# Performance work log

Hardware: AMD Instinct MI355X
Metric: run time of the kernel (lower is better)

## Reference

```python
import jax, jax.numpy as jnp
import numpy as np

B, C_IMG, H, W = 16, 512, 32, 32
C_AUD, K_LEN, N_HEADS = 512, 256, 8
HEAD_DIM = C_AUD // N_HEADS
EPS = 1e-5


def setup_inputs() -> dict:
    key = jax.random.key(0)
    ks = jax.random.split(key, 12)
    s_img = 1.0 / np.sqrt(C_IMG)
    s_aud = 1.0 / np.sqrt(C_AUD)
    return {
        "img_feat": jax.random.normal(ks[0], (B, C_IMG, H, W), jnp.float32),
        "audio_feat": jax.random.normal(ks[1], (B, K_LEN, C_AUD), jnp.float32),
        "Wq": jax.random.uniform(ks[2], (C_IMG, C_AUD), jnp.float32, -s_img, s_img),
        "bq": jnp.zeros((C_AUD,), jnp.float32),
        "Wk": jax.random.uniform(ks[3], (C_AUD, C_AUD), jnp.float32, -s_aud, s_aud),
        "bk": jnp.zeros((C_AUD,), jnp.float32),
        "Wv": jax.random.uniform(ks[4], (C_AUD, C_AUD), jnp.float32, -s_aud, s_aud),
        "bv": jnp.zeros((C_AUD,), jnp.float32),
        "Wo": jax.random.uniform(ks[5], (C_AUD, C_IMG), jnp.float32, -s_aud, s_aud),
        "bo": jnp.zeros((C_IMG,), jnp.float32),
        "gamma": jnp.ones((C_IMG,), jnp.float32),
        "beta": jnp.zeros((C_IMG,), jnp.float32),
    }


def reference(img_feat, audio_feat, Wq, bq, Wk, bk, Wv, bv, Wo, bo, gamma, beta):
    b, c, h, w = img_feat.shape
    # b c h w -> b (h w) c
    img_seq = img_feat.reshape(b, c, h * w).transpose(0, 2, 1)
    q = img_seq @ Wq + bq                      # [b, q, C_AUD]
    k = audio_feat @ Wk + bk                   # [b, k, C_AUD]
    v = audio_feat @ Wv + bv
    # split heads: b s (h d) -> b h s d
    def split(x):
        bs, s, _ = x.shape
        return x.reshape(bs, s, N_HEADS, HEAD_DIM).transpose(0, 2, 1, 3)
    qh, kh, vh = split(q), split(k), split(v)
    scale = HEAD_DIM ** -0.5
    scores = jnp.einsum('bhqd,bhkd->bhqk', qh, kh) * scale
    weights = jax.nn.softmax(scores, axis=-1)
    attn = jnp.einsum('bhqk,bhkd->bhqd', weights, vh)
    attn = attn.transpose(0, 2, 1, 3).reshape(b, h * w, C_AUD)
    proj = attn @ Wo + bo                      # [b, q, C_IMG]
    y = img_seq + proj
    mu = jnp.mean(y, axis=-1, keepdims=True)
    var = jnp.mean((y - mu) ** 2, axis=-1, keepdims=True)
    y = (y - mu) * jax.lax.rsqrt(var + EPS) * gamma + beta
    # b (h w) c -> b c h w
    return y.transpose(0, 2, 1).reshape(b, c, h, w)
```

## Files before the change

kernel.cpp:

```cpp
#include <hip/hip_runtime.h>
#include <cstddef>

#define B_SZ 16
#define HW 1024
#define CCH 512
#define K_LEN 256
#define N_HEADS 8
#define EPS 1e-5f

typedef __bf16 bf16;
typedef bf16 bf16x8 __attribute__((ext_vector_type(8)));
typedef bf16 bf16x4 __attribute__((ext_vector_type(4)));
typedef float f32x4 __attribute__((ext_vector_type(4)));

__device__ __forceinline__ void gl_lds16(const bf16* g, bf16* l) {
    __builtin_amdgcn_global_load_lds(
        (const __attribute__((address_space(1))) void*)g,
        (__attribute__((address_space(3))) void*)l, 16, 0, 0);
}

__global__ __launch_bounds__(256) void transpose_cast_img(
    const float* __restrict__ src, bf16* __restrict__ dst)
{
    const int b  = blockIdx.z;
    const int s0 = blockIdx.x * 64;
    const int c0 = blockIdx.y * 64;
    __shared__ bf16 T[64][72];
    const int tid = threadIdx.x;
    {
        const int r = tid >> 2, cs = (tid & 3) << 4;
        const float* sp = src + ((size_t)b * CCH + c0 + r) * HW + s0 + cs;
        #pragma unroll
        for (int i = 0; i < 4; ++i) {
            float4 f = *(const float4*)(sp + i * 4);
            T[r][cs + i*4 + 0] = (bf16)f.x;
            T[r][cs + i*4 + 1] = (bf16)f.y;
            T[r][cs + i*4 + 2] = (bf16)f.z;
            T[r][cs + i*4 + 3] = (bf16)f.w;
        }
    }
    __syncthreads();
    {
        const int ss = tid >> 2, ks = (tid & 3) << 4;
        bf16x8 a, b8;
        #pragma unroll
        for (int j = 0; j < 8; ++j) { a[j] = T[ks + j][ss]; b8[j] = T[ks + 8 + j][ss]; }
        bf16* dp = dst + ((size_t)b * HW + s0 + ss) * CCH + c0 + ks;
        *(bf16x8*)dp = a;
        *(bf16x8*)(dp + 8) = b8;
    }
}

__global__ __launch_bounds__(256) void transpose_cast_w(
    const float* __restrict__ Wq, const float* __restrict__ Wk,
    const float* __restrict__ Wv, const float* __restrict__ Wo,
    bf16* __restrict__ dst)
{
    const int w = blockIdx.z;
    const float* src = (w == 0) ? Wq : (w == 1) ? Wk : (w == 2) ? Wv : Wo;
    const int n0 = blockIdx.x * 64;
    const int k0 = blockIdx.y * 64;
    __shared__ bf16 T[64][72];
    const int tid = threadIdx.x;
    {
        const int r = tid >> 2, cs = (tid & 3) << 4;
        const float* sp = src + (size_t)(k0 + r) * CCH + n0 + cs;
        #pragma unroll
        for (int i = 0; i < 4; ++i) {
            float4 f = *(const float4*)(sp + i * 4);
            T[r][cs + i*4 + 0] = (bf16)f.x;
            T[r][cs + i*4 + 1] = (bf16)f.y;
            T[r][cs + i*4 + 2] = (bf16)f.z;
            T[r][cs + i*4 + 3] = (bf16)f.w;
        }
    }
    __syncthreads();
    {
        const int nn = tid >> 2, ks = (tid & 3) << 4;
        bf16x8 a, b8;
        #pragma unroll
        for (int j = 0; j < 8; ++j) { a[j] = T[ks + j][nn]; b8[j] = T[ks + 8 + j][nn]; }
        bf16* dp = dst + (size_t)w * CCH * CCH + (size_t)(n0 + nn) * CCH + k0 + ks;
        *(bf16x8*)dp = a;
        *(bf16x8*)(dp + 8) = b8;
    }
}

__global__ __launch_bounds__(256) void cast_audio(
    const float* __restrict__ src, bf16* __restrict__ dst)
{
    const size_t i = ((size_t)blockIdx.x * 256 + threadIdx.x) * 8;
    float4 a = *(const float4*)(src + i);
    float4 b = *(const float4*)(src + i + 4);
    bf16x8 o;
    o[0] = (bf16)a.x; o[1] = (bf16)a.y; o[2] = (bf16)a.z; o[3] = (bf16)a.w;
    o[4] = (bf16)b.x; o[5] = (bf16)b.y; o[6] = (bf16)b.z; o[7] = (bf16)b.w;
    *(bf16x8*)(dst + i) = o;
}

__global__ __launch_bounds__(256) void gemm_bf16_mfma(
    const bf16* __restrict__ A, const bf16* __restrict__ Bt,
    const float* __restrict__ bias, bf16* __restrict__ out)
{
    const int tid  = threadIdx.x;
    const int wave = tid >> 6, lane = tid & 63;
    const int m0 = blockIdx.x * 128;
    const int n0 = blockIdx.y * 128;
    const int l15 = lane & 15, quad = lane >> 4;
    const int wm = (wave >> 1) * 64, wn = (wave & 1) * 64;

    __shared__ bf16 As[128 * 32];
    __shared__ bf16 Bs[128 * 32];

    const int r16 = lane >> 2;
    const int ks  = (lane & 3) * 8;

    f32x4 acc[4][4];
    #pragma unroll
    for (int i = 0; i < 4; ++i)
        #pragma unroll
        for (int j = 0; j < 4; ++j)
            acc[i][j] = (f32x4){0.f, 0.f, 0.f, 0.f};

    for (int k0 = 0; k0 < 512; k0 += 32) {
        #pragma unroll
        for (int i = 0; i < 2; ++i) {
            const int c = wave * 2 + i;
            gl_lds16(A  + (size_t)(m0 + c * 16 + r16) * 512 + k0 + ks, &As[c * 512]);
            gl_lds16(Bt + (size_t)(n0 + c * 16 + r16) * 512 + k0 + ks, &Bs[c * 512]);
        }
        __syncthreads();
        bf16x8 af[4], bfr[4];
        #pragma unroll
        for (int i = 0; i < 4; ++i)
            af[i] = *(const bf16x8*)&As[(wm + i * 16 + l15) * 32 + quad * 8];
        #pragma unroll
        for (int j = 0; j < 4; ++j)
            bfr[j] = *(const bf16x8*)&Bs[(wn + j * 16 + l15) * 32 + quad * 8];
        #pragma unroll
        for (int i = 0; i < 4; ++i)
            #pragma unroll
            for (int j = 0; j < 4; ++j)
                acc[i][j] = __builtin_amdgcn_mfma_f32_16x16x32_bf16(bfr[j], af[i], acc[i][j], 0, 0, 0);
        __syncthreads();
    }

    #pragma unroll
    for (int j = 0; j < 4; ++j) {
        const int gn = n0 + wn + j * 16 + quad * 4;
        const float4 bv4 = *(const float4*)(bias + gn);
        const float bb[4] = {bv4.x, bv4.y, bv4.z, bv4.w};
        #pragma unroll
        for (int i = 0; i < 4; ++i) {
            const int gm = m0 + wm + i * 16 + l15;
            bf16x4 ov;
            #pragma unroll
            for (int r = 0; r < 4; ++r) ov[r] = (bf16)(acc[i][j][r] + bb[r]);
            *(bf16x4*)(out + (size_t)gm * 512 + gn) = ov;
        }
    }
}

__global__ __launch_bounds__(256) void gemm_kv_mfma(
    const bf16* __restrict__ A, const bf16* __restrict__ Bt,
    const float* __restrict__ bk, const float* __restrict__ bv,
    bf16* __restrict__ khout, bf16* __restrict__ vtout)
{
    const int tid  = threadIdx.x;
    const int wave = tid >> 6, lane = tid & 63;
    const int m0 = blockIdx.x * 128;
    const int n0 = blockIdx.y * 128;
    const int l15 = lane & 15, quad = lane >> 4;
    const int wm = (wave >> 1) * 64, wn = (wave & 1) * 64;

    __shared__ bf16 As[128 * 32];
    __shared__ bf16 Bs[128 * 32];

    const int r16 = lane >> 2;
    const int ks  = (lane & 3) * 8;

    f32x4 acc[4][4];
    #pragma unroll
    for (int i = 0; i < 4; ++i)
        #pragma unroll
        for (int j = 0; j < 4; ++j)
            acc[i][j] = (f32x4){0.f, 0.f, 0.f, 0.f};

    for (int k0 = 0; k0 < 512; k0 += 32) {
        #pragma unroll
        for (int i = 0; i < 2; ++i) {
            const int c = wave * 2 + i;
            gl_lds16(A  + (size_t)(m0 + c * 16 + r16) * 512 + k0 + ks, &As[c * 512]);
            gl_lds16(Bt + (size_t)(n0 + c * 16 + r16) * 512 + k0 + ks, &Bs[c * 512]);
        }
        __syncthreads();
        bf16x8 af[4], bfr[4];
        #pragma unroll
        for (int i = 0; i < 4; ++i)
            af[i] = *(const bf16x8*)&As[(wm + i * 16 + l15) * 32 + quad * 8];
        #pragma unroll
        for (int j = 0; j < 4; ++j)
            bfr[j] = *(const bf16x8*)&Bs[(wn + j * 16 + l15) * 32 + quad * 8];
        #pragma unroll
        for (int i = 0; i < 4; ++i)
            #pragma unroll
            for (int j = 0; j < 4; ++j)
                acc[i][j] = __builtin_amdgcn_mfma_f32_16x16x32_bf16(af[i], bfr[j], acc[i][j], 0, 0, 0);
        __syncthreads();
    }

    #pragma unroll
    for (int j = 0; j < 4; ++j) {
        const int gn = n0 + wn + j * 16 + l15;
        if (gn < 512) {
            const int h = gn >> 6, d = gn & 63;
            const float bias = bk[gn];
            #pragma unroll
            for (int i = 0; i < 4; ++i) {
                const int gm = m0 + wm + i * 16 + quad * 4;
                const int b = gm >> 8, key = gm & 255;
                bf16* base = khout + ((((size_t)b * N_HEADS + h) * K_LEN) + key) * 64 + d;
                #pragma unroll
                for (int r = 0; r < 4; ++r)
                    base[(size_t)r * 64] = (bf16)(acc[i][j][r] + bias);
            }
        } else {
            const int ch = gn - 512;
            const int h = ch >> 6, d = ch & 63;
            const float bias = bv[ch];
            #pragma unroll
            for (int i = 0; i < 4; ++i) {
                const int gm = m0 + wm + i * 16 + quad * 4;
                const int b = gm >> 8, key = gm & 255;
                bf16x4 pk;
                #pragma unroll
                for (int r = 0; r < 4; ++r) pk[r] = (bf16)(acc[i][j][r] + bias);
                *(bf16x4*)(vtout + (((size_t)b * N_HEADS + h) * 64 + d) * K_LEN + key) = pk;
            }
        }
    }
}

__global__ __launch_bounds__(256) void attn_mfma(
    const bf16* __restrict__ q,
    const bf16* __restrict__ kh,
    const bf16* __restrict__ vt,
    bf16* __restrict__ o)
{
    const int bh = blockIdx.x;
    const int s0 = blockIdx.y * 64;
    const int tid = threadIdx.x;
    const int wave = tid >> 6, lane = tid & 63;
    const int l15 = lane & 15, quad = lane >> 4;
    const int b = bh >> 3, h = bh & 7;

    __shared__ bf16 KsPt[18432];
    __shared__ bf16 Vs[16896];

    const bf16* khb = kh + (size_t)bh * K_LEN * 64;
    const bf16* vtb = vt + (size_t)bh * 64 * K_LEN;

    #pragma unroll
    for (int i = 0; i < 8; ++i) {
        const int chunk = tid + (i << 8);
        const int key = chunk >> 3, dseg = (chunk & 7) << 3;
        *(bf16x8*)&KsPt[key * 72 + dseg] = *(const bf16x8*)(khb + key * 64 + dseg);
        const int d = chunk >> 5, kseg = (chunk & 31) << 3;
        *(bf16x8*)&Vs[d * 264 + kseg] = *(const bf16x8*)(vtb + d * 256 + kseg);
    }
    __syncthreads();

    const int qrow = s0 + wave * 16 + l15;
    const bf16* qp = q + ((size_t)(b * HW + qrow)) * 512 + h * 64 + quad * 8;
    const bf16x8 qf0 = *(const bf16x8*)qp;
    const bf16x8 qf1 = *(const bf16x8*)(qp + 32);

    f32x4 acc[16];
    #pragma unroll
    for (int m = 0; m < 16; ++m) acc[m] = (f32x4){0.f, 0.f, 0.f, 0.f};
    #pragma unroll
    for (int m = 0; m < 16; ++m) {
        const bf16x8 a0 = *(const bf16x8*)&KsPt[(m * 16 + l15) * 72 + quad * 8];
        const bf16x8 a1 = *(const bf16x8*)&KsPt[(m * 16 + l15) * 72 + 32 + quad * 8];
        acc[m] = __builtin_amdgcn_mfma_f32_16x16x32_bf16(a0, qf0, acc[m], 0, 0, 0);
        acc[m] = __builtin_amdgcn_mfma_f32_16x16x32_bf16(a1, qf1, acc[m], 0, 0, 0);
    }

    float mx = -1e30f;
    #pragma unroll
    for (int m = 0; m < 16; ++m)
        mx = fmaxf(mx, fmaxf(fmaxf(acc[m][0], acc[m][1]), fmaxf(acc[m][2], acc[m][3])));
    mx = fmaxf(mx, __shfl_xor(mx, 16, 64));
    mx = fmaxf(mx, __shfl_xor(mx, 32, 64));

    __syncthreads();

    bf16* PtW = &KsPt[wave * 4224];
    float l_sum = 0.f;
    #pragma unroll
    for (int m = 0; m < 16; ++m) {
        bf16x4 pk;
        #pragma unroll
        for (int r = 0; r < 4; ++r) {
            const float p = __expf((acc[m][r] - mx) * 0.125f);
            l_sum += p;
            pk[r] = (bf16)p;
        }
        *(bf16x4*)&PtW[l15 * 264 + m * 16 + quad * 4] = pk;
    }
    l_sum += __shfl_xor(l_sum, 16, 64);
    l_sum += __shfl_xor(l_sum, 32, 64);
    __syncthreads();

    f32x4 oacc[4];
    #pragma unroll
    for (int m = 0; m < 4; ++m) oacc[m] = (f32x4){0.f, 0.f, 0.f, 0.f};
    #pragma unroll
    for (int s = 0; s < 8; ++s) {
        const bf16x8 pb = *(const bf16x8*)&PtW[l15 * 264 + s * 32 + quad * 8];
        #pragma unroll
        for (int m = 0; m < 4; ++m) {
            const bf16x8 va = *(const bf16x8*)&Vs[(m * 16 + l15) * 264 + s * 32 + quad * 8];
            oacc[m] = __builtin_amdgcn_mfma_f32_16x16x32_bf16(va, pb, oacc[m], 0, 0, 0);
        }
    }

    const float inv = 1.0f / l_sum;
    bf16* op = o + ((size_t)(b * HW + qrow)) * 512 + h * 64 + quad * 4;
    #pragma unroll
    for (int m = 0; m < 4; ++m) {
        bf16x4 ov;
        #pragma unroll
        for (int r = 0; r < 4; ++r) ov[r] = (bf16)(oacc[m][r] * inv);
        *(bf16x4*)&op[m * 16] = ov;
    }
}

__global__ __launch_bounds__(256) void ln_kernel(
    const bf16* __restrict__ proj, const bf16* __restrict__ imgb,
    const float* __restrict__ gamma, const float* __restrict__ beta,
    float* __restrict__ out)
{
    const int b  = blockIdx.y;
    const int s0 = blockIdx.x * 32;
    const int tid = threadIdx.x;
    const int wave = tid >> 6, lane = tid & 63;

    __shared__ float Y[32][513];

    const int cb = lane * 8;
    const float4 g0 = *(const float4*)(gamma + cb);
    const float4 g1 = *(const float4*)(gamma + cb + 4);
    const float4 b0 = *(const float4*)(beta + cb);
    const float4 b1 = *(const float4*)(beta + cb + 4);
    const float gg[8] = {g0.x, g0.y, g0.z, g0.w, g1.x, g1.y, g1.z, g1.w};
    const float bb[8] = {b0.x, b0.y, b0.z, b0.w, b1.x, b1.y, b1.z, b1.w};

    #pragma unroll
    for (int rr = 0; rr < 8; ++rr) {
        const int ss = wave * 8 + rr;
        const size_t row = (size_t)b * HW + s0 + ss;
        bf16x8 p8 = *(const bf16x8*)(proj + row * 512 + cb);
        bf16x8 i8 = *(const bf16x8*)(imgb + row * 512 + cb);
        float y[8];
        float sum = 0.f, sq = 0.f;
        #pragma unroll
        for (int j = 0; j < 8; ++j) {
            y[j] = (float)p8[j] + (float)i8[j];
            sum += y[j]; sq += y[j] * y[j];
        }
        #pragma unroll
        for (int off = 32; off > 0; off >>= 1) {
            sum += __shfl_xor(sum, off, 64);
            sq  += __shfl_xor(sq, off, 64);
        }
        const float mu = sum * (1.f / 512.f);
        const float rs = rsqrtf(sq * (1.f / 512.f) - mu * mu + EPS);
        #pragma unroll
        for (int j = 0; j < 8; ++j)
            Y[ss][cb + j] = (y[j] - mu) * rs * gg[j] + bb[j];
    }
    __syncthreads();

    #pragma unroll
    for (int it = 0; it < 16; ++it) {
        const int idx = it * 256 + tid;
        const int c = idx >> 3, sseg = (idx & 7) << 2;
        float4 o4;
        o4.x = Y[sseg + 0][c];
        o4.y = Y[sseg + 1][c];
        o4.z = Y[sseg + 2][c];
        o4.w = Y[sseg + 3][c];
        *(float4*)(out + ((size_t)b * CCH + c) * HW + s0 + sseg) = o4;
    }
}

extern "C" void kernel_launch(void* const* d_in, const int* in_sizes, int n_in,
                              void* d_out, int out_size, void* d_ws, size_t ws_size,
                              hipStream_t stream) {
    const float* img   = (const float*)d_in[0];
    const float* audio = (const float*)d_in[1];
    const float* Wq    = (const float*)d_in[2];
    const float* bq    = (const float*)d_in[3];
    const float* Wk    = (const float*)d_in[4];
    const float* bk    = (const float*)d_in[5];
    const float* Wv    = (const float*)d_in[6];
    const float* bv    = (const float*)d_in[7];
    const float* Wo    = (const float*)d_in[8];
    const float* bo    = (const float*)d_in[9];
    const float* gamma = (const float*)d_in[10];
    const float* beta  = (const float*)d_in[11];

    bf16* wsb    = (bf16*)d_ws;
    bf16* img_bf = wsb;
    bf16* aud_bf = img_bf + 8388608;
    bf16* wT     = aud_bf + 2097152;
    bf16* q_bf   = wT + 1048576;
    bf16* kh_bf  = q_bf + 8388608;
    bf16* vt_bf  = kh_bf + 2097152;
    bf16* a_bf   = vt_bf + 2097152;
    bf16* p_bf   = q_bf;

    transpose_cast_img<<<dim3(16, 8, 16), 256, 0, stream>>>(img, img_bf);
    cast_audio<<<dim3(1024), 256, 0, stream>>>(audio, aud_bf);
    transpose_cast_w<<<dim3(8, 8, 4), 256, 0, stream>>>(Wq, Wk, Wv, Wo, wT);

    gemm_bf16_mfma<<<dim3(128, 4), 256, 0, stream>>>(img_bf, wT, bq, q_bf);
    gemm_kv_mfma<<<dim3(32, 8), 256, 0, stream>>>(aud_bf, wT + 262144, bk, bv, kh_bf, vt_bf);
    attn_mfma<<<dim3(B_SZ * N_HEADS, HW / 64), 256, 0, stream>>>(q_bf, kh_bf, vt_bf, a_bf);
    gemm_bf16_mfma<<<dim3(128, 4), 256, 0, stream>>>(a_bf, wT + 3 * 262144, bo, p_bf);
    ln_kernel<<<dim3(32, 16), 256, 0, stream>>>(p_bf, img_bf, gamma, beta, (float*)d_out);
}
```

Before: 198.0 us.

## Fuse output projection GEMM with residual add and LayerNorm epilogue

Replaces the separate output-projection GEMM and LayerNorm kernels with one kernel. Each 512-thread block computes a 64-row by full 512-column tile, so whole rows are resident for the LayerNorm statistics, which are reduced across waves through shared memory. The result is transposed through LDS and written out in NCHW layout. This removes the bf16 intermediate write and read and one launch, but only 256 blocks are launched, there is no double buffering of the K loop, and the per-thread accumulator count is high.

```diff
diff --git a/kernel.cpp b/kernel.cpp
--- a/kernel.cpp
+++ b/kernel.cpp
@@ -336,62 +336,140 @@
     }
 }
 
-__global__ __launch_bounds__(256) void ln_kernel(
-    const bf16* __restrict__ proj, const bf16* __restrict__ imgb,
+__global__ __launch_bounds__(512, 2) void gemm_o_ln(
+    const bf16* __restrict__ A,
+    const bf16* __restrict__ Bt,
+    const float* __restrict__ bo,
+    const bf16* __restrict__ imgb,
     const float* __restrict__ gamma, const float* __restrict__ beta,
     float* __restrict__ out)
 {
-    const int b  = blockIdx.y;
-    const int s0 = blockIdx.x * 32;
-    const int tid = threadIdx.x;
+    const int tid  = threadIdx.x;
     const int wave = tid >> 6, lane = tid & 63;
-
-    __shared__ float Y[32][513];
-
-    const int cb = lane * 8;
-    const float4 g0 = *(const float4*)(gamma + cb);
-    const float4 g1 = *(const float4*)(gamma + cb + 4);
-    const float4 b0 = *(const float4*)(beta + cb);
-    const float4 b1 = *(const float4*)(beta + cb + 4);
-    const float gg[8] = {g0.x, g0.y, g0.z, g0.w, g1.x, g1.y, g1.z, g1.w};
-    const float bb[8] = {b0.x, b0.y, b0.z, b0.w, b1.x, b1.y, b1.z, b1.w};
-
-    #pragma unroll
-    for (int rr = 0; rr < 8; ++rr) {
-        const int ss = wave * 8 + rr;
-        const size_t row = (size_t)b * HW + s0 + ss;
-        bf16x8 p8 = *(const bf16x8*)(proj + row * 512 + cb);
-        bf16x8 i8 = *(const bf16x8*)(imgb + row * 512 + cb);
-        float y[8];
-        float sum = 0.f, sq = 0.f;
-        #pragma unroll
-        for (int j = 0; j < 8; ++j) {
-            y[j] = (float)p8[j] + (float)i8[j];
-            sum += y[j]; sq += y[j] * y[j];
-        }
-        #pragma unroll
-        for (int off = 32; off > 0; off >>= 1) {
-            sum += __shfl_xor(sum, off, 64);
-            sq  += __shfl_xor(sq, off, 64);
-        }
-        const float mu = sum * (1.f / 512.f);
-        const float rs = rsqrtf(sq * (1.f / 512.f) - mu * mu + EPS);
-        #pragma unroll
-        for (int j = 0; j < 8; ++j)
-            Y[ss][cb + j] = (y[j] - mu) * rs * gg[j] + bb[j];
+    const int l15 = lane & 15, quad = lane >> 4;
+    const int m0 = blockIdx.x * 64;
+    const int wn = wave * 64;
+
+    __shared__ bf16 As[64 * 32];
+    __shared__ union {
+        bf16  Bs[512 * 32];
+        float Y[16][513];
+    } u;
+    __shared__ float2 Ps[64][9];
+
+    const int r16 = lane >> 2;
+    const int ks  = (lane & 3) * 8;
+
+    f32x4 acc[4][4];
+    #pragma unroll
+    for (int i = 0; i < 4; ++i)
+        #pragma unroll
+        for (int j = 0; j < 4; ++j)
+            acc[i][j] = (f32x4){0.f, 0.f, 0.f, 0.f};
+
+    for (int k0 = 0; k0 < 512; k0 += 32) {
+        if (wave < 4)
+            gl_lds16(A + (size_t)(m0 + wave * 16 + r16) * 512 + k0 + ks, &As[wave * 512]);
+        #pragma unroll
+        for (int i = 0; i < 4; ++i) {
+            const int cc = wave * 4 + i;
+            gl_lds16(Bt + (size_t)(cc * 16 + r16) * 512 + k0 + ks, &u.Bs[cc * 512]);
+        }
+        __syncthreads();
+        bf16x8 af[4], bfr[4];
+        #pragma unroll
+        for (int i = 0; i < 4; ++i)
+            af[i] = *(const bf16x8*)&As[(i * 16 + l15) * 32 + quad * 8];
+        #pragma unroll
+        for (int j = 0; j < 4; ++j)
+            bfr[j] = *(const bf16x8*)&u.Bs[(wn + j * 16 + l15) * 32 + quad * 8];
+        #pragma unroll
+        for (int i = 0; i < 4; ++i)
+            #pragma unroll
+            for (int j = 0; j < 4; ++j)
+                acc[i][j] = __builtin_amdgcn_mfma_f32_16x16x32_bf16(bfr[j], af[i], acc[i][j], 0, 0, 0);
+        __syncthreads();
+    }
+
+    float sm[4], sq[4];
+    #pragma unroll
+    for (int i = 0; i < 4; ++i) {
+        float s = 0.f, q2 = 0.f;
+        const size_t row = (size_t)(m0 + i * 16 + l15);
+        #pragma unroll
+        for (int j = 0; j < 4; ++j) {
+            const int c = wn + j * 16 + quad * 4;
+            const float4 b4 = *(const float4*)(bo + c);
+            const float bb[4] = {b4.x, b4.y, b4.z, b4.w};
+            const bf16x4 r4 = *(const bf16x4*)(imgb + row * 512 + c);
+            #pragma unroll
+            for (int r = 0; r < 4; ++r) {
+                const float y = acc[i][j][r] + bb[r] + (float)r4[r];
+                acc[i][j][r] = y;
+                s += y; q2 += y * y;
+            }
+        }
+        s  += __shfl_xor(s, 16, 64);  s  += __shfl_xor(s, 32, 64);
+        q2 += __shfl_xor(q2, 16, 64); q2 += __shfl_xor(q2, 32, 64);
+        sm[i] = s; sq[i] = q2;
+    }
+    if (quad == 0) {
+        #pragma unroll
+        for (int i = 0; i < 4; ++i)
+            Ps[i * 16 + l15][wave] = make_float2(sm[i], sq[i]);
     }
     __syncthreads();
 
-    #pragma unroll
-    for (int it = 0; it < 16; ++it) {
-        const int idx = it * 256 + tid;
-        const int c = idx >> 3, sseg = (idx & 7) << 2;
-        float4 o4;
-        o4.x = Y[sseg + 0][c];
-        o4.y = Y[sseg + 1][c];
-        o4.z = Y[sseg + 2][c];
-        o4.w = Y[sseg + 3][c];
-        *(float4*)(out + ((size_t)b * CCH + c) * HW + s0 + sseg) = o4;
+    float mu[4], rs[4];
+    #pragma unroll
+    for (int i = 0; i < 4; ++i) {
+        float s = 0.f, q2 = 0.f;
+        #pragma unroll
+        for (int w = 0; w < 8; ++w) {
+            const float2 p = Ps[i * 16 + l15][w];
+            s += p.x; q2 += p.y;
+        }
+        const float m = s * (1.f / 512.f);
+        mu[i] = m;
+        rs[i] = rsqrtf(q2 * (1.f / 512.f) - m * m + EPS);
+    }
+
+    float gg[4][4], be[4][4];
+    #pragma unroll
+    for (int j = 0; j < 4; ++j) {
+        const int c = wn + j * 16 + quad * 4;
+        const float4 g4 = *(const float4*)(gamma + c);
+        const float4 e4 = *(const float4*)(beta + c);
+        gg[j][0] = g4.x; gg[j][1] = g4.y; gg[j][2] = g4.z; gg[j][3] = g4.w;
+        be[j][0] = e4.x; be[j][1] = e4.y; be[j][2] = e4.z; be[j][3] = e4.w;
+    }
+
+    const int b  = m0 >> 10;
+    const int s0 = m0 & 1023;
+
+    for (int i = 0; i < 4; ++i) {
+        __syncthreads();
+        #pragma unroll
+        for (int j = 0; j < 4; ++j) {
+            float4 o4;
+            o4.x = (acc[i][j][0] - mu[i]) * rs[i] * gg[j][0] + be[j][0];
+            o4.y = (acc[i][j][1] - mu[i]) * rs[i] * gg[j][1] + be[j][1];
+            o4.z = (acc[i][j][2] - mu[i]) * rs[i] * gg[j][2] + be[j][2];
+            o4.w = (acc[i][j][3] - mu[i]) * rs[i] * gg[j][3] + be[j][3];
+            *(float4*)&u.Y[l15][wn + j * 16 + quad * 4] = o4;
+        }
+        __syncthreads();
+        #pragma unroll
+        for (int it = 0; it < 4; ++it) {
+            const int idx = it * 512 + tid;
+            const int c = idx >> 2, ss = (idx & 3) << 2;
+            float4 o4;
+            o4.x = u.Y[ss + 0][c];
+            o4.y = u.Y[ss + 1][c];
+            o4.z = u.Y[ss + 2][c];
+            o4.w = u.Y[ss + 3][c];
+            *(float4*)(out + ((size_t)b * CCH + c) * HW + s0 + i * 16 + ss) = o4;
+        }
     }
 }
 
@@ -419,7 +497,6 @@
     bf16* kh_bf  = q_bf + 8388608;
     bf16* vt_bf  = kh_bf + 2097152;
     bf16* a_bf   = vt_bf + 2097152;
-    bf16* p_bf   = q_bf;
 
     transpose_cast_img<<<dim3(16, 8, 16), 256, 0, stream>>>(img, img_bf);
     cast_audio<<<dim3(1024), 256, 0, stream>>>(audio, aud_bf);
@@ -428,6 +505,5 @@
     gemm_bf16_mfma<<<dim3(128, 4), 256, 0, stream>>>(img_bf, wT, bq, q_bf);
     gemm_kv_mfma<<<dim3(32, 8), 256, 0, stream>>>(aud_bf, wT + 262144, bk, bv, kh_bf, vt_bf);
     attn_mfma<<<dim3(B_SZ * N_HEADS, HW / 64), 256, 0, stream>>>(q_bf, kh_bf, vt_bf, a_bf);
-    gemm_bf16_mfma<<<dim3(128, 4), 256, 0, stream>>>(a_bf, wT + 3 * 262144, bo, p_bf);
-    ln_kernel<<<dim3(32, 16), 256, 0, stream>>>(p_bf, img_bf, gamma, beta, (float*)d_out);
-}
+    gemm_o_ln<<<dim3(256), 512, 0, stream>>>(a_bf, wT + 3 * 262144, bo, img_bf, gamma, beta, (float*)d_out);
+}
```

Result: slower. 211.7 us (+6.9%).
